# Kernel tuning notes

Hardware: AMD Instinct MI355X
Metric: run time of the kernel (lower is better)

The kernel has to match this reference:

```python
import jax, jax.numpy as jnp
import numpy as np

N_NODES = 50000
N_EDGES = 800000
D_IN = 128
D_OUT = 128


def _gcn_conv(x, W, b, src, dst, num_nodes):
    """PyG GCNConv: h = x @ W^T; symmetric-normalized mean over neighbors
    (with self-loops); out = aggregate + bias.
    src/dst already include self-loops."""
    h = x @ W.T  # [N, C_out]
    ones = jnp.ones(dst.shape[0], dtype=x.dtype)
    deg = jax.ops.segment_sum(ones, dst, num_segments=num_nodes)  # in-degree incl self-loop
    deg_inv_sqrt = jnp.where(deg > 0, jax.lax.rsqrt(deg), 0.0)
    norm = deg_inv_sqrt[src] * deg_inv_sqrt[dst]  # [E+N]
    msgs = h[src] * norm[:, None]  # gather + scale
    out = jax.ops.segment_sum(msgs, dst, num_segments=num_nodes)  # scatter-add
    return out + b


def setup_inputs() -> dict:
    key = jax.random.key(0)
    ks = jax.random.split(key, 9)
    x_r1 = jax.random.normal(ks[0], (N_NODES, D_IN), dtype=jnp.float32)
    x_r2 = jax.random.normal(ks[1], (N_NODES, D_IN), dtype=jnp.float32)
    x_i1 = jax.random.normal(ks[2], (N_NODES, D_IN), dtype=jnp.float32)
    x_i2 = jax.random.normal(ks[3], (N_NODES, D_IN), dtype=jnp.float32)
    edge_index = jax.random.randint(ks[4], (2, N_EDGES), 0, N_NODES, dtype=jnp.int64)
    s = 1.0 / np.sqrt(D_IN)
    W1 = jax.random.uniform(ks[5], (D_OUT, D_IN), minval=-s, maxval=s, dtype=jnp.float32)
    W2 = jax.random.uniform(ks[6], (D_OUT, D_IN), minval=-s, maxval=s, dtype=jnp.float32)
    b1 = jax.random.uniform(ks[7], (D_OUT,), minval=-s, maxval=s, dtype=jnp.float32)
    b2 = jax.random.uniform(ks[8], (D_OUT,), minval=-s, maxval=s, dtype=jnp.float32)
    return {"x_r1": x_r1, "x_r2": x_r2, "x_i1": x_i1, "x_i2": x_i2,
            "edge_index": edge_index, "W1": W1, "b1": b1, "W2": W2, "b2": b2}


def reference(x_r1, x_r2, x_i1, x_i2, edge_index, W1, b1, W2, b2):
    num_nodes = x_r1.shape[0]
    loops = jnp.arange(num_nodes, dtype=edge_index.dtype)
    src = jnp.concatenate([edge_index[0], loops])  # add self-loops
    dst = jnp.concatenate([edge_index[1], loops])
    # real1/imag1 share (W1, b1); real2/imag2 share (W2, b2)
    h_r1 = _gcn_conv(x_r1, W1, b1, src, dst, num_nodes)
    h_r2 = _gcn_conv(x_r2, W2, b2, src, dst, num_nodes)
    h_i1 = _gcn_conv(x_i1, W1, b1, src, dst, num_nodes)
    h_i2 = _gcn_conv(x_i2, W2, b2, src, dst, num_nodes)
    return (h_r1, h_r2, h_i1, h_i2)
```

## Files before the change

### kernel.cpp

```cpp
#include <hip/hip_runtime.h>

#define DD 128
#define PARTS 4
#define SLICES 16
#define PBINS 12544

typedef __bf16 bf16x8 __attribute__((ext_vector_type(8)));
typedef float f32x4 __attribute__((ext_vector_type(4)));

static __device__ __forceinline__ unsigned short f2bf(float f) {
    unsigned int u = __float_as_uint(f);
    u += 0x7FFF + ((u >> 16) & 1);
    return (unsigned short)(u >> 16);
}


__global__ __launch_bounds__(1024) void k_count(
    const int* __restrict__ dst, int* __restrict__ partial,
    const float* __restrict__ W1, const float* __restrict__ W2,
    unsigned short* __restrict__ wbf, int N, int E)
{
    const int bid = blockIdx.x;
    const int tid = threadIdx.x;
    if (bid >= PARTS * SLICES) {
        int i = (bid - PARTS * SLICES) * 1024 + tid;
        float4 v = (i < 4096) ? ((const float4*)W1)[i] : ((const float4*)W2)[i - 4096];
        ushort4 b;
        b.x = f2bf(v.x); b.y = f2bf(v.y); b.z = f2bf(v.z); b.w = f2bf(v.w);
        *(ushort4*)&wbf[(size_t)i * 4] = b;
        return;
    }

    __shared__ int hist[PBINS];
    const int p     = bid & (PARTS - 1);
    const int c     = bid / PARTS;
    const int psize = (N + PARTS - 1) / PARTS;
    const int lo    = p * psize;

    for (int t = tid; t < psize; t += 1024) hist[t] = 0;
    __syncthreads();

    const int sl = (E + SLICES - 1) / SLICES;
    const int e0 = c * sl;
    const int e1 = (e0 + sl < E) ? e0 + sl : E;

    int e = e0 + tid * 4;
    for (; e + 3 < e1; e += 4096) {
        int4 d = *(const int4*)&dst[e];
        unsigned t0 = (unsigned)(d.x - lo), t1 = (unsigned)(d.y - lo);
        unsigned t2 = (unsigned)(d.z - lo), t3 = (unsigned)(d.w - lo);
        if (t0 < (unsigned)psize) atomicAdd(&hist[t0], 1);
        if (t1 < (unsigned)psize) atomicAdd(&hist[t1], 1);
        if (t2 < (unsigned)psize) atomicAdd(&hist[t2], 1);
        if (t3 < (unsigned)psize) atomicAdd(&hist[t3], 1);
    }
    if (e < e1) {
        for (int k = e; k < e1; ++k) {
            unsigned t0 = (unsigned)(dst[k] - lo);
            if (t0 < (unsigned)psize) atomicAdd(&hist[t0], 1);
        }
    }
    __syncthreads();

    int* op = partial + (size_t)c * N;
    for (int t = tid; t < psize; t += 1024) {
        int g = lo + t;
        if (g < N) op[g] = hist[t];
    }
}


__global__ __launch_bounds__(1024) void k_scan1(const int* __restrict__ partial,
                                                int* __restrict__ rp,
                                                float* __restrict__ dinv,
                                                int* __restrict__ cur,
                                                int* __restrict__ bsum, int N) {
    __shared__ int wsum[16];
    const int tid = threadIdx.x, lane = tid & 63, wid = tid >> 6;
    const int i = blockIdx.x * 1024 + tid;
    int v = 0;
    if (i < N) {
#pragma unroll
        for (int c = 0; c < SLICES; ++c) v += partial[c * N + i];
    }
    int s = v;
    for (int off = 1; off < 64; off <<= 1) {
        int t = __shfl_up(s, off, 64);
        if (lane >= off) s += t;
    }
    if (lane == 63) wsum[wid] = s;
    __syncthreads();
    int woff = 0, total = 0;
#pragma unroll
    for (int w2 = 0; w2 < 16; ++w2) {
        int t = wsum[w2];
        if (w2 < wid) woff += t;
        total += t;
    }
    if (i < N) {
        rp[i + 1] = woff + s;
        dinv[i] = rsqrtf((float)(v + 1));
        cur[i] = v;
    }
    if (tid == 0) bsum[blockIdx.x] = total;
}

__global__ __launch_bounds__(1024) void k_scan2(const int* __restrict__ bsum,
                                                int* __restrict__ rp, int N) {
    __shared__ int boff_s;
    const int tid = threadIdx.x;
    if (tid < 64) {
        int v = (tid < (int)blockIdx.x) ? bsum[tid] : 0;
        for (int off = 32; off > 0; off >>= 1) v += __shfl_down(v, off, 64);
        if (tid == 0) boff_s = v;
    }
    __syncthreads();
    const int i = blockIdx.x * 1024 + tid;
    if (i < N) rp[i + 1] += boff_s;
    if (i == 0) rp[0] = 0;
}


__global__ __launch_bounds__(512) void k_mid(
    const float* __restrict__ x0, const float* __restrict__ x1,
    const float* __restrict__ x2, const float* __restrict__ x3,
    const unsigned short* __restrict__ wbf,
    unsigned short* __restrict__ h,
    const int* __restrict__ ei, const int* __restrict__ rp,
    int* __restrict__ cur, const float* __restrict__ dinv,
    int2* __restrict__ csr,
    int N, int E, int GB)
{
    const int bid = blockIdx.x;
    const int tid = threadIdx.x;

    if (bid >= GB) {
        int e2 = ((bid - GB) * 512 + tid) * 2;
        if (e2 >= E) return;
        int2 s = *(const int2*)&ei[e2];
        int2 d = *(const int2*)&ei[E + e2];
        int o0 = atomicSub(&cur[d.x], 1);
        csr[rp[d.x] + o0 - 1] = make_int2(s.x, __float_as_int(dinv[s.x]));
        int o1 = atomicSub(&cur[d.y], 1);
        csr[rp[d.y] + o1 - 1] = make_int2(s.y, __float_as_int(dinv[s.y]));
        return;
    }

    const int m = bid & 3;
    const float* x = (m == 0) ? x0 : (m == 1) ? x1 : (m == 2) ? x2 : x3;
    const unsigned short* Wg = wbf + (size_t)(m & 1) * 128 * 128;

    __shared__ unsigned short smem[128 * 136];

    const int n0   = (bid >> 2) * 128;
    const int w    = tid >> 6;
    const int lane = tid & 63;
    const int am   = lane & 15;
    const int aq   = lane >> 4;
    const int r0   = w * 16;

    int arow = n0 + r0 + am; if (arow > N - 1) arow = N - 1;
    const float* xr = x + (size_t)arow * DD + aq * 8;
    float4 a0[4], a1[4];
#pragma unroll
    for (int q = 0; q < 4; ++q) {
        a0[q] = *(const float4*)(xr + q * 32);
        a1[q] = *(const float4*)(xr + q * 32 + 4);
    }

#pragma unroll
    for (int t = tid; t < 2048; t += 512)
        ((uint4*)smem)[t ^ ((t >> 4) & 7)] = ((const uint4*)Wg)[t];
    __syncthreads();

    bf16x8 afr[4];
#pragma unroll
    for (int q = 0; q < 4; ++q) {
        afr[q][0] = (__bf16)a0[q].x; afr[q][1] = (__bf16)a0[q].y;
        afr[q][2] = (__bf16)a0[q].z; afr[q][3] = (__bf16)a0[q].w;
        afr[q][4] = (__bf16)a1[q].x; afr[q][5] = (__bf16)a1[q].y;
        afr[q][6] = (__bf16)a1[q].z; afr[q][7] = (__bf16)a1[q].w;
    }

    f32x4 acc[8] = {};
#pragma unroll
    for (int q = 0; q < 4; ++q) {
        const int kc = q * 32 + aq * 8;
#pragma unroll
        for (int ct = 0; ct < 8; ++ct) {
            bf16x8 bf = *(const bf16x8*)&smem[(ct * 16 + am) * 128 +
                                              (kc ^ ((am & 7) << 3))];
            acc[ct] = __builtin_amdgcn_mfma_f32_16x16x32_bf16(afr[q], bf, acc[ct], 0, 0, 0);
        }
    }
    __syncthreads();

    const int cc = lane & 15;
    const int rr = (lane >> 4) * 4;
#pragma unroll
    for (int ct = 0; ct < 8; ++ct)
#pragma unroll
        for (int i = 0; i < 4; ++i)
            smem[(r0 + rr + i) * 136 + ct * 16 + cc] = f2bf(acc[ct][i]);
    __syncthreads();

#pragma unroll
    for (int k = 0; k < 4; ++k) {
        int f = k * 512 + tid;
        int row2 = f >> 4, ch = f & 15;
        int n = n0 + row2;
        if (n < N)
            *(uint4*)(h + ((size_t)n * 4 + m) * DD + ch * 8) =
                *(const uint4*)&smem[row2 * 136 + ch * 8];
    }
}


static __device__ __forceinline__ void acc8(float* a, uint4 v, float wt) {
    a[0] += __uint_as_float(v.x << 16) * wt;
    a[1] += __uint_as_float(v.x & 0xffff0000u) * wt;
    a[2] += __uint_as_float(v.y << 16) * wt;
    a[3] += __uint_as_float(v.y & 0xffff0000u) * wt;
    a[4] += __uint_as_float(v.z << 16) * wt;
    a[5] += __uint_as_float(v.z & 0xffff0000u) * wt;
    a[6] += __uint_as_float(v.w << 16) * wt;
    a[7] += __uint_as_float(v.w & 0xffff0000u) * wt;
}

__global__ __launch_bounds__(256) void k_gather(
    const int* __restrict__ rp, const int2* __restrict__ csr,
    const float* __restrict__ dinv, const unsigned short* __restrict__ h,
    const float* __restrict__ b1, const float* __restrict__ b2,
    float* __restrict__ out, int N)
{
    const int n = blockIdx.x * 4 + (threadIdx.x >> 6);
    if (n >= N) return;
    const int lane = threadIdx.x & 63;
    const int m    = lane >> 4;
    const int c    = (lane & 15) * 8;
    const size_t off = (size_t)lane * 8;

    const float dn = dinv[n];
    float a[8];

    {
        const float sn = dn * dn;
        const float* bb = (m & 1) ? b2 : b1;
        uint4 hv = *(const uint4*)(h + (size_t)n * 512 + off);
        float4 bv0 = *(const float4*)(bb + c);
        float4 bv1 = *(const float4*)(bb + c + 4);
        a[0] = bv0.x; a[1] = bv0.y; a[2] = bv0.z; a[3] = bv0.w;
        a[4] = bv1.x; a[5] = bv1.y; a[6] = bv1.z; a[7] = bv1.w;
        acc8(a, hv, sn);
    }

    int jb = rp[n];
    const int j1 = rp[n + 1];

    for (; jb + 7 < j1; jb += 8) {
        int2 e0 = csr[jb],     e1 = csr[jb + 1], e2 = csr[jb + 2], e3 = csr[jb + 3];
        int2 e4 = csr[jb + 4], e5 = csr[jb + 5], e6 = csr[jb + 6], e7 = csr[jb + 7];
        float w0 = __int_as_float(e0.y) * dn, w1 = __int_as_float(e1.y) * dn,
              w2 = __int_as_float(e2.y) * dn, w3 = __int_as_float(e3.y) * dn,
              w4 = __int_as_float(e4.y) * dn, w5 = __int_as_float(e5.y) * dn,
              w6 = __int_as_float(e6.y) * dn, w7 = __int_as_float(e7.y) * dn;
        uint4 v0 = *(const uint4*)(h + (size_t)e0.x * 512 + off);
        uint4 v1 = *(const uint4*)(h + (size_t)e1.x * 512 + off);
        uint4 v2 = *(const uint4*)(h + (size_t)e2.x * 512 + off);
        uint4 v3 = *(const uint4*)(h + (size_t)e3.x * 512 + off);
        uint4 v4 = *(const uint4*)(h + (size_t)e4.x * 512 + off);
        uint4 v5 = *(const uint4*)(h + (size_t)e5.x * 512 + off);
        uint4 v6 = *(const uint4*)(h + (size_t)e6.x * 512 + off);
        uint4 v7 = *(const uint4*)(h + (size_t)e7.x * 512 + off);
        acc8(a, v0, w0); acc8(a, v1, w1); acc8(a, v2, w2); acc8(a, v3, w3);
        acc8(a, v4, w4); acc8(a, v5, w5); acc8(a, v6, w6); acc8(a, v7, w7);
    }
    if (jb < j1) {
        const int last = j1 - 1;
#pragma unroll
        for (int k = 0; k < 8; ++k) {
            int idx = jb + k;
            int2 e = csr[idx <= last ? idx : last];
            float wt = (idx <= last) ? __int_as_float(e.y) * dn : 0.f;
            uint4 v = *(const uint4*)(h + (size_t)e.x * 512 + off);
            acc8(a, v, wt);
        }
    }

    float* po = out + ((size_t)m * N + n) * DD + c;
    f32x4 r0, r1;
    r0.x = a[0]; r0.y = a[1]; r0.z = a[2]; r0.w = a[3];
    r1.x = a[4]; r1.y = a[5]; r1.z = a[6]; r1.w = a[7];
    __builtin_nontemporal_store(r0, (f32x4*)po);
    __builtin_nontemporal_store(r1, (f32x4*)(po + 4));
}


extern "C" void kernel_launch(void* const* d_in, const int* in_sizes, int n_in,
                              void* d_out, int out_size, void* d_ws, size_t ws_size,
                              hipStream_t stream) {
    const float* x0 = (const float*)d_in[0];
    const float* x1 = (const float*)d_in[1];
    const float* x2 = (const float*)d_in[2];
    const float* x3 = (const float*)d_in[3];
    const int*   ei = (const int*)d_in[4];
    const float* W1 = (const float*)d_in[5];
    const float* b1 = (const float*)d_in[6];
    const float* W2 = (const float*)d_in[7];
    const float* b2 = (const float*)d_in[8];
    float* out = (float*)d_out;

    const int N = in_sizes[0] / DD;
    const int E = in_sizes[4] / 2;

    int*   cur  = (int*)d_ws;
    int*   rp   = cur + 65536;
    float* dinv = (float*)(rp + 65536);
    int*   bsum = (int*)(dinv + 65536);
    unsigned short* wbf = (unsigned short*)(bsum + 256);
    int2*  csr  = (int2*)(wbf + 2 * 128 * 128);
    unsigned short* h = (unsigned short*)(csr + E);

    int* partial = (int*)csr;

    const int nscan = (N + 1023) / 1024;
    const int GB    = ((N + 127) / 128) * 4;
    const int FB    = (E / 2 + 511) / 512;

    k_count<<<PARTS * SLICES + 8, 1024, 0, stream>>>(ei + E, partial, W1, W2, wbf, N, E);
    k_scan1<<<nscan, 1024, 0, stream>>>(partial, rp, dinv, cur, bsum, N);
    k_scan2<<<nscan, 1024, 0, stream>>>(bsum, rp, N);
    k_mid  <<<GB + FB, 512, 0, stream>>>(x0, x1, x2, x3, wbf, h,
                                         ei, rp, cur, dinv, csr, N, E, GB);
    k_gather<<<(N + 3) / 4, 256, 0, stream>>>(rp, csr, dinv, h, b1, b2, out, N);
}
```

Measured before the change: 370.0 us.

## Fill CSR via per-partition LDS cursors instead of global atomics

The CSR fill now mirrors the count pass. Each (partition, slice) block loads per-node write cursors (row pointer plus a per-slice exclusive prefix computed in scan1) into shared memory and claims slots with LDS atomics, replacing global atomicSub on a cursor array. Partitions double from 4 to 8 so the cursor table fits alongside the GEMM's shared buffer, and the partial counts move into the output buffer as scratch. The cost is that every fill block rereads the whole edge slice, so edge reads grow with the partition count, and the fill now runs as only 128 blocks placed before the GEMM blocks.

```diff
diff --git a/kernel.cpp b/kernel.cpp
--- a/kernel.cpp
+++ b/kernel.cpp
@@ -1,9 +1,10 @@
 #include <hip/hip_runtime.h>
 
 #define DD 128
-#define PARTS 4
+#define PARTS 8
 #define SLICES 16
-#define PBINS 12544
+#define PBINS 6272
+#define FB (PARTS * SLICES)
 
 typedef __bf16 bf16x8 __attribute__((ext_vector_type(8)));
 typedef float f32x4 __attribute__((ext_vector_type(4)));
@@ -22,8 +23,8 @@
 {
     const int bid = blockIdx.x;
     const int tid = threadIdx.x;
-    if (bid >= PARTS * SLICES) {
-        int i = (bid - PARTS * SLICES) * 1024 + tid;
+    if (bid >= FB) {
+        int i = (bid - FB) * 1024 + tid;
         float4 v = (i < 4096) ? ((const float4*)W1)[i] : ((const float4*)W2)[i - 4096];
         ushort4 b;
         b.x = f2bf(v.x); b.y = f2bf(v.y); b.z = f2bf(v.z); b.w = f2bf(v.w);
@@ -70,18 +71,23 @@
 }
 
 
-__global__ __launch_bounds__(1024) void k_scan1(const int* __restrict__ partial,
+__global__ __launch_bounds__(1024) void k_scan1(int* __restrict__ partial,
                                                 int* __restrict__ rp,
                                                 float* __restrict__ dinv,
-                                                int* __restrict__ cur,
                                                 int* __restrict__ bsum, int N) {
     __shared__ int wsum[16];
     const int tid = threadIdx.x, lane = tid & 63, wid = tid >> 6;
     const int i = blockIdx.x * 1024 + tid;
     int v = 0;
     if (i < N) {
-#pragma unroll
-        for (int c = 0; c < SLICES; ++c) v += partial[c * N + i];
+        int run = 0;
+#pragma unroll
+        for (int c = 0; c < SLICES; ++c) {
+            int t = partial[(size_t)c * N + i];
+            partial[(size_t)c * N + i] = run;
+            run += t;
+        }
+        v = run;
     }
     int s = v;
     for (int off = 1; off < 64; off <<= 1) {
@@ -100,7 +106,6 @@
     if (i < N) {
         rp[i + 1] = woff + s;
         dinv[i] = rsqrtf((float)(v + 1));
-        cur[i] = v;
     }
     if (tid == 0) bsum[blockIdx.x] = total;
 }
@@ -127,32 +132,74 @@
     const unsigned short* __restrict__ wbf,
     unsigned short* __restrict__ h,
     const int* __restrict__ ei, const int* __restrict__ rp,
-    int* __restrict__ cur, const float* __restrict__ dinv,
-    int2* __restrict__ csr,
-    int N, int E, int GB)
+    const float* __restrict__ dinv, const int* __restrict__ partial,
+    int2* __restrict__ csr, int N, int E)
 {
+    __shared__ __align__(16) char smem_raw[128 * 136 * 2];
     const int bid = blockIdx.x;
     const int tid = threadIdx.x;
 
-    if (bid >= GB) {
-        int e2 = ((bid - GB) * 512 + tid) * 2;
-        if (e2 >= E) return;
-        int2 s = *(const int2*)&ei[e2];
-        int2 d = *(const int2*)&ei[E + e2];
-        int o0 = atomicSub(&cur[d.x], 1);
-        csr[rp[d.x] + o0 - 1] = make_int2(s.x, __float_as_int(dinv[s.x]));
-        int o1 = atomicSub(&cur[d.y], 1);
-        csr[rp[d.y] + o1 - 1] = make_int2(s.y, __float_as_int(dinv[s.y]));
+    if (bid < FB) {
+        int* curs = (int*)smem_raw;
+        const int p     = bid & (PARTS - 1);
+        const int c     = bid / PARTS;
+        const int psize = (N + PARTS - 1) / PARTS;
+        const int lo    = p * psize;
+
+        for (int t = tid; t < psize; t += 512) {
+            int g = lo + t;
+            curs[t] = (g < N) ? rp[g] + partial[(size_t)c * N + g] : 0;
+        }
+        __syncthreads();
+
+        const int sl = (E + SLICES - 1) / SLICES;
+        const int e0 = c * sl;
+        const int e1 = (e0 + sl < E) ? e0 + sl : E;
+
+        int e = e0 + tid * 4;
+        for (; e + 3 < e1; e += 2048) {
+            int4 d = *(const int4*)&ei[E + e];
+            int4 s = *(const int4*)&ei[e];
+            unsigned t0 = (unsigned)(d.x - lo), t1 = (unsigned)(d.y - lo);
+            unsigned t2 = (unsigned)(d.z - lo), t3 = (unsigned)(d.w - lo);
+            if (t0 < (unsigned)psize) {
+                int pos = atomicAdd(&curs[t0], 1);
+                csr[pos] = make_int2(s.x, __float_as_int(dinv[s.x]));
+            }
+            if (t1 < (unsigned)psize) {
+                int pos = atomicAdd(&curs[t1], 1);
+                csr[pos] = make_int2(s.y, __float_as_int(dinv[s.y]));
+            }
+            if (t2 < (unsigned)psize) {
+                int pos = atomicAdd(&curs[t2], 1);
+                csr[pos] = make_int2(s.z, __float_as_int(dinv[s.z]));
+            }
+            if (t3 < (unsigned)psize) {
+                int pos = atomicAdd(&curs[t3], 1);
+                csr[pos] = make_int2(s.w, __float_as_int(dinv[s.w]));
+            }
+        }
+        if (e < e1) {
+            for (int k = e; k < e1; ++k) {
+                int dk = ei[E + k];
+                unsigned t0 = (unsigned)(dk - lo);
+                if (t0 < (unsigned)psize) {
+                    int sk = ei[k];
+                    int pos = atomicAdd(&curs[t0], 1);
+                    csr[pos] = make_int2(sk, __float_as_int(dinv[sk]));
+                }
+            }
+        }
         return;
     }
 
-    const int m = bid & 3;
+    const int gb = bid - FB;
+    const int m  = gb & 3;
     const float* x = (m == 0) ? x0 : (m == 1) ? x1 : (m == 2) ? x2 : x3;
     const unsigned short* Wg = wbf + (size_t)(m & 1) * 128 * 128;
-
-    __shared__ unsigned short smem[128 * 136];
-
-    const int n0   = (bid >> 2) * 128;
+    unsigned short* smem = (unsigned short*)smem_raw;
+
+    const int n0   = (gb >> 2) * 128;
     const int w    = tid >> 6;
     const int lane = tid & 63;
     const int am   = lane & 15;
@@ -313,24 +360,22 @@
     const int N = in_sizes[0] / DD;
     const int E = in_sizes[4] / 2;
 
-    int*   cur  = (int*)d_ws;
-    int*   rp   = cur + 65536;
+    int*   rp   = (int*)d_ws;
     float* dinv = (float*)(rp + 65536);
     int*   bsum = (int*)(dinv + 65536);
     unsigned short* wbf = (unsigned short*)(bsum + 256);
     int2*  csr  = (int2*)(wbf + 2 * 128 * 128);
     unsigned short* h = (unsigned short*)(csr + E);
 
-    int* partial = (int*)csr;
+    int* partial = (int*)d_out;
 
     const int nscan = (N + 1023) / 1024;
     const int GB    = ((N + 127) / 128) * 4;
-    const int FB    = (E / 2 + 511) / 512;
-
-    k_count<<<PARTS * SLICES + 8, 1024, 0, stream>>>(ei + E, partial, W1, W2, wbf, N, E);
-    k_scan1<<<nscan, 1024, 0, stream>>>(partial, rp, dinv, cur, bsum, N);
+
+    k_count<<<FB + 8, 1024, 0, stream>>>(ei + E, partial, W1, W2, wbf, N, E);
+    k_scan1<<<nscan, 1024, 0, stream>>>(partial, rp, dinv, bsum, N);
     k_scan2<<<nscan, 1024, 0, stream>>>(bsum, rp, N);
-    k_mid  <<<GB + FB, 512, 0, stream>>>(x0, x1, x2, x3, wbf, h,
-                                         ei, rp, cur, dinv, csr, N, E, GB);
+    k_mid  <<<FB + GB, 512, 0, stream>>>(x0, x1, x2, x3, wbf, h,
+                                         ei, rp, dinv, partial, csr, N, E);
     k_gather<<<(N + 3) / 4, 256, 0, stream>>>(rp, csr, dinv, h, b1, b2, out, N);
 }
```

Measured after the change: 366.7 us. Within noise of the previous version (-0.9%).
